# Kernel tuning notes

Hardware: AMD Instinct MI355X
Metric: run time of the kernel (lower is better)

## Reference

```python
import jax, jax.numpy as jnp
import numpy as np

NEG_INF = -9.0e15  # matches torch's -9000000000000000.0 mask value
ALPHA = 0.2        # LeakyReLU negative slope


def setup_inputs() -> dict:
    key = jax.random.key(0)
    k1, k2, k3, k4 = jax.random.split(key, 4)
    N, F_in, F_out = 8192, 128, 128
    x = jax.random.normal(k1, (N, F_in), dtype=jnp.float32)
    adj = jax.random.randint(k2, (N, N), 0, 2, dtype=jnp.int32)
    W = jax.random.normal(k3, (F_in, F_out), dtype=jnp.float32) * (1.0 / np.sqrt(F_in))
    a = jax.random.normal(k4, (2 * F_out, 1), dtype=jnp.float32) * (1.0 / np.sqrt(2 * F_out))
    return {"x": x, "adj": adj, "W": W, "a": a}


def reference(x, adj, W, a):
    # h = W(input): [N, F_out]
    h = x @ W
    F_out = h.shape[1]
    # a([h_i || h_j]) = h_i . a[:F] + h_j . a[F:]  -- identical math to the
    # original NxNx2F concat, without materializing it.
    a_src = a[:F_out, 0]   # coefficients on the row (i) node
    a_dst = a[F_out:, 0]   # coefficients on the column (j) node
    s_src = h @ a_src      # [N]
    s_dst = h @ a_dst      # [N]
    e = jax.nn.leaky_relu(s_src[:, None] + s_dst[None, :], negative_slope=ALPHA)  # [N, N]
    e = jnp.where(adj > 0, e, jnp.float32(NEG_INF))
    attention = jax.nn.softmax(e, axis=1)
    # dropout omitted (identity at eval) for a deterministic baseline
    h_prime = attention @ h  # [N, F_out]
    return h_prime
```

## Files before the change

### kernel.cpp

```cpp
#include <hip/hip_runtime.h>

#define N 8192
#define F 128
#define ALPHA 0.2f

typedef __attribute__((ext_vector_type(8))) short short8;
typedef __attribute__((ext_vector_type(4))) float f32x4;
typedef unsigned short u16;

__device__ __forceinline__ u16 f2bf(float f) {
    unsigned int u = __float_as_uint(f);
    u += 0x7fff + ((u >> 16) & 1);
    return (u16)(u >> 16);
}
__device__ __forceinline__ float bf2f(u16 b) {
    return __uint_as_float(((unsigned int)b) << 16);
}
__device__ __forceinline__ float lrelu(float z) { return fmaxf(z, ALPHA * z); }

__global__ __launch_bounds__(256) void gemm_h(const float* __restrict__ x,
                                              const float* __restrict__ W,
                                              const float* __restrict__ aa,
                                              u16* __restrict__ hT,
                                              float* __restrict__ ssrc,
                                              float* __restrict__ sdst) {
    __shared__ float xs[32 * 128];
    __shared__ float Wsh[32 * 128];
    const int t = threadIdx.x;
    const int i0 = blockIdx.x * 32;
    const int c4 = (t & 31) * 4;
    const int r8 = t >> 5;

#pragma unroll
    for (int p = 0; p < 4; ++p) {
        int rr = p * 8 + r8;
        *(float4*)&xs[rr * 128 + c4] = *(const float4*)&x[(size_t)(i0 + rr) * 128 + c4];
    }

    const int tx = t & 31, ty = t >> 5;
    const int r0 = ty * 4, c0 = tx * 4;
    float acc[4][4] = {};

    for (int kc = 0; kc < 4; ++kc) {
        __syncthreads();
#pragma unroll
        for (int p = 0; p < 4; ++p) {
            int k = p * 8 + r8;
            *(float4*)&Wsh[k * 128 + c4] = *(const float4*)&W[(kc * 32 + k) * 128 + c4];
        }
        __syncthreads();
#pragma unroll 4
        for (int k = 0; k < 32; k += 4) {
            float xr[4][4];
#pragma unroll
            for (int rr = 0; rr < 4; ++rr)
                *(float4*)xr[rr] = *(const float4*)&xs[(r0 + rr) * 128 + kc * 32 + k];
#pragma unroll
            for (int kk = 0; kk < 4; ++kk) {
                float4 wv = *(const float4*)&Wsh[(k + kk) * 128 + c0];
#pragma unroll
                for (int rr = 0; rr < 4; ++rr) {
                    acc[rr][0] += xr[rr][kk] * wv.x;
                    acc[rr][1] += xr[rr][kk] * wv.y;
                    acc[rr][2] += xr[rr][kk] * wv.z;
                    acc[rr][3] += xr[rr][kk] * wv.w;
                }
            }
        }
    }

#pragma unroll
    for (int rr = 0; rr < 4; ++rr)
#pragma unroll
        for (int cc = 0; cc < 4; ++cc)
            hT[(size_t)(c0 + cc) * N + (i0 + r0 + rr)] = f2bf(acc[rr][cc]);

    float4 asv = *(const float4*)&aa[c0];
    float4 adv = *(const float4*)&aa[F + c0];
#pragma unroll
    for (int rr = 0; rr < 4; ++rr) {
        float vs = acc[rr][0] * asv.x + acc[rr][1] * asv.y + acc[rr][2] * asv.z + acc[rr][3] * asv.w;
        float vd = acc[rr][0] * adv.x + acc[rr][1] * adv.y + acc[rr][2] * adv.z + acc[rr][3] * adv.w;
#pragma unroll
        for (int off = 16; off >= 1; off >>= 1) {
            vs += __shfl_down(vs, off, 32);
            vd += __shfl_down(vd, off, 32);
        }
        if (tx == 0) {
            ssrc[i0 + r0 + rr] = vs;
            sdst[i0 + r0 + rr] = vd;
        }
    }
}

__global__ __launch_bounds__(256, 2) void attn_mfma(const int* __restrict__ adj,
                                                    const u16* __restrict__ hT,
                                                    const float* __restrict__ ssrc,
                                                    const float* __restrict__ sdst,
                                                    float* __restrict__ out,
                                                    float* __restrict__ pacc1,
                                                    float* __restrict__ pS) {
    __shared__ short8 wsh[2][4][64];
    __shared__ float srow[2][2][16];

    const int t = threadIdx.x;
    const int w = t >> 6, L = t & 63;
    const int quad = L >> 4, l16 = L & 15;
    const int i0 = blockIdx.x * 32;
    const int split = blockIdx.y;
    const int jbase = split * (N / 2);
    const int NC = (N / 2) / 64;

    const int rt = w & 1, ks = w >> 1;
    const int fragid = rt * 2 + ks;
    const int prow = i0 + rt * 16 + l16;
    const float s_i = ssrc[prow];

    const int* pA = adj + (size_t)prow * N + jbase + ks * 32 + quad * 8;
    const float* pD = sdst + jbase + ks * 32 + quad * 8;
    const u16* pB = hT + (size_t)(w * 32 + l16) * N + jbase + quad * 8;

    f32x4 acc[2][2];
#pragma unroll
    for (int a = 0; a < 2; ++a)
#pragma unroll
        for (int b = 0; b < 2; ++b) acc[a][b] = 0.f;
    float rsum = 0.f;

    auto compute_write = [&](int buf, int4 a0, int4 a1, float4 d0, float4 d1) {
        int m[8] = {a0.x, a0.y, a0.z, a0.w, a1.x, a1.y, a1.z, a1.w};
        float d[8] = {d0.x, d0.y, d0.z, d0.w, d1.x, d1.y, d1.z, d1.w};
        short8 pk;
        float s = 0.f;
#pragma unroll
        for (int k = 0; k < 8; ++k) {
            float e = __expf(lrelu(s_i + d[k]));
            float wv = (m[k] > 0) ? e : 0.f;
            u16 b = f2bf(wv);
            s += bf2f(b);
            pk[k] = (short)b;
        }
        rsum += s;
        wsh[buf][fragid][L] = pk;
    };

    int4 aC0 = *(const int4*)(pA);
    int4 aC1 = *(const int4*)(pA + 4);
    float4 dC0 = *(const float4*)(pD);
    float4 dC1 = *(const float4*)(pD + 4);
    compute_write(0, aC0, aC1, dC0, dC1);

    short8 Bbuf[2][2];
#pragma unroll
    for (int c2 = 0; c2 < 2; ++c2)
#pragma unroll
        for (int kb = 0; kb < 2; ++kb)
            Bbuf[c2][kb] = *(const short8*)(pB + (size_t)c2 * 16 * N + kb * 32);

    int4 aN0 = *(const int4*)(pA + 64);
    int4 aN1 = *(const int4*)(pA + 64 + 4);
    float4 dN0 = *(const float4*)(pD + 64);
    float4 dN1 = *(const float4*)(pD + 64 + 4);

    for (int c = 1; c < NC; ++c) {
        __syncthreads();
        const int coff = c * 64;

        short8 Bload[2][2];
#pragma unroll
        for (int c2 = 0; c2 < 2; ++c2)
#pragma unroll
            for (int kb = 0; kb < 2; ++kb)
                Bload[c2][kb] = *(const short8*)(pB + (size_t)c2 * 16 * N + kb * 32 + coff);

        const int cn = (c + 1 < NC) ? c + 1 : NC - 1;
        int4 aP0 = *(const int4*)(pA + cn * 64);
        int4 aP1 = *(const int4*)(pA + cn * 64 + 4);
        float4 dP0 = *(const float4*)(pD + cn * 64);
        float4 dP1 = *(const float4*)(pD + cn * 64 + 4);

        short8 af[4];
#pragma unroll
        for (int fs = 0; fs < 4; ++fs) af[fs] = wsh[(c - 1) & 1][fs][L];
#pragma unroll
        for (int c2 = 0; c2 < 2; ++c2)
#pragma unroll
            for (int rc = 0; rc < 2; ++rc)
#pragma unroll
                for (int kb = 0; kb < 2; ++kb)
                    acc[c2][rc] = __builtin_amdgcn_mfma_f32_16x16x32_bf16(
                        af[rc * 2 + kb], Bbuf[c2][kb], acc[c2][rc], 0, 0, 0);

        compute_write(c & 1, aN0, aN1, dN0, dN1);

        aN0 = aP0; aN1 = aP1; dN0 = dP0; dN1 = dP1;
#pragma unroll
        for (int c2 = 0; c2 < 2; ++c2)
#pragma unroll
            for (int kb = 0; kb < 2; ++kb) Bbuf[c2][kb] = Bload[c2][kb];
    }

    __syncthreads();
    {
        short8 af[4];
#pragma unroll
        for (int fs = 0; fs < 4; ++fs) af[fs] = wsh[(NC - 1) & 1][fs][L];
#pragma unroll
        for (int c2 = 0; c2 < 2; ++c2)
#pragma unroll
            for (int rc = 0; rc < 2; ++rc)
#pragma unroll
                for (int kb = 0; kb < 2; ++kb)
                    acc[c2][rc] = __builtin_amdgcn_mfma_f32_16x16x32_bf16(
                        af[rc * 2 + kb], Bbuf[c2][kb], acc[c2][rc], 0, 0, 0);
    }

    float* dst = split ? pacc1 : out;
#pragma unroll
    for (int c2 = 0; c2 < 2; ++c2) {
        const int col = (w * 2 + c2) * 16 + l16;
#pragma unroll
        for (int rc = 0; rc < 2; ++rc) {
            const int row0 = i0 + rc * 16 + quad * 4;
#pragma unroll
            for (int r = 0; r < 4; ++r)
                dst[(size_t)(row0 + r) * F + col] = acc[c2][rc][r];
        }
    }

    rsum += __shfl_xor(rsum, 16);
    rsum += __shfl_xor(rsum, 32);
    if (L < 16) srow[rt][ks][l16] = rsum;
    __syncthreads();
    if (t < 32) pS[split * N + i0 + t] = srow[t >> 4][0][t & 15] + srow[t >> 4][1][t & 15];
}

__global__ __launch_bounds__(256) void finalize(float* __restrict__ out,
                                                const float* __restrict__ pacc1,
                                                const float* __restrict__ pS) {
    const int idx = (blockIdx.x * 256 + threadIdx.x) * 4;
    const int i = idx >> 7;
    const float inv = 1.0f / (pS[i] + pS[N + i]);
    float4 a0 = *(const float4*)&out[idx];
    float4 a1 = *(const float4*)&pacc1[idx];
    float4 o = {(a0.x + a1.x) * inv, (a0.y + a1.y) * inv,
                (a0.z + a1.z) * inv, (a0.w + a1.w) * inv};
    *(float4*)&out[idx] = o;
}

extern "C" void kernel_launch(void* const* d_in, const int* in_sizes, int n_in,
                              void* d_out, int out_size, void* d_ws, size_t ws_size,
                              hipStream_t stream) {
    (void)in_sizes; (void)n_in; (void)out_size; (void)ws_size;
    const float* x   = (const float*)d_in[0];
    const int*   adj = (const int*)d_in[1];
    const float* W   = (const float*)d_in[2];
    const float* a   = (const float*)d_in[3];
    float* out = (float*)d_out;

    u16* hT     = (u16*)d_ws;
    float* ssrc = (float*)(hT + (size_t)N * F);
    float* sdst = ssrc + N;
    float* pS   = sdst + N;
    float* pacc1 = pS + 2 * N;

    gemm_h<<<N / 32, 256, 0, stream>>>(x, W, a, hT, ssrc, sdst);
    attn_mfma<<<dim3(N / 32, 2), 256, 0, stream>>>(adj, hT, ssrc, sdst, out, pacc1, pS);
    finalize<<<(N * F / 4) / 256, 256, 0, stream>>>(out, pacc1, pS);
}
```

Measured before the change: 413.4 us.

## Restructure attention kernel: per-wave row tiles, 8-way key split, no LDS

The attention kernel is rewritten so each wave owns 16 rows and all 128 output columns. Each wave computes its own bf16 attention weights in registers and feeds them straight into MFMA, which removes the shared-memory staging and block barriers. The key dimension is split 8 ways instead of 2, and occupancy is raised to 4 blocks per SM, with a two-deep register prefetch of adj and sdst. In exchange, finalize must now reduce 8 partial accumulators, which adds workspace traffic, and each wave re-reads the hT tiles that were previously shared across the block.

```diff
diff --git a/kernel.cpp b/kernel.cpp
--- a/kernel.cpp
+++ b/kernel.cpp
@@ -2,6 +2,10 @@
 
 #define N 8192
 #define F 128
+#define NS 8
+#define JC (N / NS)
+#define CK 32
+#define NC (JC / CK)
 #define ALPHA 0.2f
 
 typedef __attribute__((ext_vector_type(8))) short short8;
@@ -93,158 +97,118 @@
     }
 }
 
-__global__ __launch_bounds__(256, 2) void attn_mfma(const int* __restrict__ adj,
+__global__ __launch_bounds__(256, 4) void attn_mfma(const int* __restrict__ adj,
                                                     const u16* __restrict__ hT,
                                                     const float* __restrict__ ssrc,
                                                     const float* __restrict__ sdst,
-                                                    float* __restrict__ out,
-                                                    float* __restrict__ pacc1,
+                                                    float* __restrict__ pacc,
                                                     float* __restrict__ pS) {
-    __shared__ short8 wsh[2][4][64];
-    __shared__ float srow[2][2][16];
-
     const int t = threadIdx.x;
     const int w = t >> 6, L = t & 63;
     const int quad = L >> 4, l16 = L & 15;
-    const int i0 = blockIdx.x * 32;
+    const int i0 = blockIdx.x * 64 + w * 16;
     const int split = blockIdx.y;
-    const int jbase = split * (N / 2);
-    const int NC = (N / 2) / 64;
-
-    const int rt = w & 1, ks = w >> 1;
-    const int fragid = rt * 2 + ks;
-    const int prow = i0 + rt * 16 + l16;
-    const float s_i = ssrc[prow];
-
-    const int* pA = adj + (size_t)prow * N + jbase + ks * 32 + quad * 8;
-    const float* pD = sdst + jbase + ks * 32 + quad * 8;
-    const u16* pB = hT + (size_t)(w * 32 + l16) * N + jbase + quad * 8;
-
-    f32x4 acc[2][2];
-#pragma unroll
-    for (int a = 0; a < 2; ++a)
-#pragma unroll
-        for (int b = 0; b < 2; ++b) acc[a][b] = 0.f;
+    const int jbase = split * JC;
+
+    const int row = i0 + l16;
+    const float s_i = ssrc[row];
+    const int* pA = adj + (size_t)row * N + jbase + quad * 8;
+    const float* pD = sdst + jbase + quad * 8;
+    const u16* pB = hT + (size_t)l16 * N + jbase + quad * 8;
+
+    f32x4 acc[8];
+#pragma unroll
+    for (int cg = 0; cg < 8; ++cg) acc[cg] = 0.f;
     float rsum = 0.f;
 
-    auto compute_write = [&](int buf, int4 a0, int4 a1, float4 d0, float4 d1) {
-        int m[8] = {a0.x, a0.y, a0.z, a0.w, a1.x, a1.y, a1.z, a1.w};
-        float d[8] = {d0.x, d0.y, d0.z, d0.w, d1.x, d1.y, d1.z, d1.w};
-        short8 pk;
-        float s = 0.f;
-#pragma unroll
-        for (int k = 0; k < 8; ++k) {
-            float e = __expf(lrelu(s_i + d[k]));
-            float wv = (m[k] > 0) ? e : 0.f;
-            u16 b = f2bf(wv);
-            s += bf2f(b);
-            pk[k] = (short)b;
-        }
-        rsum += s;
-        wsh[buf][fragid][L] = pk;
-    };
-
-    int4 aC0 = *(const int4*)(pA);
-    int4 aC1 = *(const int4*)(pA + 4);
-    float4 dC0 = *(const float4*)(pD);
-    float4 dC1 = *(const float4*)(pD + 4);
-    compute_write(0, aC0, aC1, dC0, dC1);
-
-    short8 Bbuf[2][2];
-#pragma unroll
-    for (int c2 = 0; c2 < 2; ++c2)
-#pragma unroll
-        for (int kb = 0; kb < 2; ++kb)
-            Bbuf[c2][kb] = *(const short8*)(pB + (size_t)c2 * 16 * N + kb * 32);
-
-    int4 aN0 = *(const int4*)(pA + 64);
-    int4 aN1 = *(const int4*)(pA + 64 + 4);
-    float4 dN0 = *(const float4*)(pD + 64);
-    float4 dN1 = *(const float4*)(pD + 64 + 4);
-
-    for (int c = 1; c < NC; ++c) {
-        __syncthreads();
-        const int coff = c * 64;
-
-        short8 Bload[2][2];
-#pragma unroll
-        for (int c2 = 0; c2 < 2; ++c2)
-#pragma unroll
-            for (int kb = 0; kb < 2; ++kb)
-                Bload[c2][kb] = *(const short8*)(pB + (size_t)c2 * 16 * N + kb * 32 + coff);
-
-        const int cn = (c + 1 < NC) ? c + 1 : NC - 1;
-        int4 aP0 = *(const int4*)(pA + cn * 64);
-        int4 aP1 = *(const int4*)(pA + cn * 64 + 4);
-        float4 dP0 = *(const float4*)(pD + cn * 64);
-        float4 dP1 = *(const float4*)(pD + cn * 64 + 4);
-
-        short8 af[4];
-#pragma unroll
-        for (int fs = 0; fs < 4; ++fs) af[fs] = wsh[(c - 1) & 1][fs][L];
-#pragma unroll
-        for (int c2 = 0; c2 < 2; ++c2)
-#pragma unroll
-            for (int rc = 0; rc < 2; ++rc)
-#pragma unroll
-                for (int kb = 0; kb < 2; ++kb)
-                    acc[c2][rc] = __builtin_amdgcn_mfma_f32_16x16x32_bf16(
-                        af[rc * 2 + kb], Bbuf[c2][kb], acc[c2][rc], 0, 0, 0);
-
-        compute_write(c & 1, aN0, aN1, dN0, dN1);
-
-        aN0 = aP0; aN1 = aP1; dN0 = dP0; dN1 = dP1;
-#pragma unroll
-        for (int c2 = 0; c2 < 2; ++c2)
-#pragma unroll
-            for (int kb = 0; kb < 2; ++kb) Bbuf[c2][kb] = Bload[c2][kb];
-    }
-
-    __syncthreads();
-    {
-        short8 af[4];
-#pragma unroll
-        for (int fs = 0; fs < 4; ++fs) af[fs] = wsh[(NC - 1) & 1][fs][L];
-#pragma unroll
-        for (int c2 = 0; c2 < 2; ++c2)
-#pragma unroll
-            for (int rc = 0; rc < 2; ++rc)
-#pragma unroll
-                for (int kb = 0; kb < 2; ++kb)
-                    acc[c2][rc] = __builtin_amdgcn_mfma_f32_16x16x32_bf16(
-                        af[rc * 2 + kb], Bbuf[c2][kb], acc[c2][rc], 0, 0, 0);
-    }
-
-    float* dst = split ? pacc1 : out;
-#pragma unroll
-    for (int c2 = 0; c2 < 2; ++c2) {
-        const int col = (w * 2 + c2) * 16 + l16;
-#pragma unroll
-        for (int rc = 0; rc < 2; ++rc) {
-            const int row0 = i0 + rc * 16 + quad * 4;
-#pragma unroll
-            for (int r = 0; r < 4; ++r)
-                dst[(size_t)(row0 + r) * F + col] = acc[c2][rc][r];
-        }
+    int4 aj[2][2];
+    float4 sd[2][2];
+    aj[0][0] = *(const int4*)(pA);
+    aj[0][1] = *(const int4*)(pA + 4);
+    sd[0][0] = *(const float4*)(pD);
+    sd[0][1] = *(const float4*)(pD + 4);
+    aj[1][0] = *(const int4*)(pA + CK);
+    aj[1][1] = *(const int4*)(pA + CK + 4);
+    sd[1][0] = *(const float4*)(pD + CK);
+    sd[1][1] = *(const float4*)(pD + CK + 4);
+
+#pragma unroll 2
+    for (int c = 0; c < NC; ++c) {
+        const int s = c & 1;
+        const int off = c * CK;
+
+        short8 B0[4];
+#pragma unroll
+        for (int cg = 0; cg < 4; ++cg)
+            B0[cg] = *(const short8*)(pB + (size_t)cg * 16 * N + off);
+
+        short8 wf;
+        {
+            int m[8] = {aj[s][0].x, aj[s][0].y, aj[s][0].z, aj[s][0].w,
+                        aj[s][1].x, aj[s][1].y, aj[s][1].z, aj[s][1].w};
+            float d[8] = {sd[s][0].x, sd[s][0].y, sd[s][0].z, sd[s][0].w,
+                          sd[s][1].x, sd[s][1].y, sd[s][1].z, sd[s][1].w};
+#pragma unroll
+            for (int k = 0; k < 8; ++k) {
+                float e = __expf(lrelu(s_i + d[k]));
+                float wv = (m[k] > 0) ? e : 0.f;
+                u16 b = f2bf(wv);
+                rsum += bf2f(b);
+                wf[k] = (short)b;
+            }
+        }
+
+        const int cp = (c + 2 < NC) ? c + 2 : c;
+        const int offp = cp * CK;
+        aj[s][0] = *(const int4*)(pA + offp);
+        aj[s][1] = *(const int4*)(pA + offp + 4);
+        sd[s][0] = *(const float4*)(pD + offp);
+        sd[s][1] = *(const float4*)(pD + offp + 4);
+
+        short8 B1[4];
+#pragma unroll
+        for (int cg = 0; cg < 4; ++cg)
+            B1[cg] = *(const short8*)(pB + (size_t)(cg + 4) * 16 * N + off);
+
+#pragma unroll
+        for (int cg = 0; cg < 4; ++cg)
+            acc[cg] = __builtin_amdgcn_mfma_f32_16x16x32_bf16(wf, B0[cg], acc[cg], 0, 0, 0);
+#pragma unroll
+        for (int cg = 0; cg < 4; ++cg)
+            acc[cg + 4] = __builtin_amdgcn_mfma_f32_16x16x32_bf16(wf, B1[cg], acc[cg + 4], 0, 0, 0);
+    }
+
+    float* dst = pacc + (size_t)split * N * F;
+#pragma unroll
+    for (int cg = 0; cg < 8; ++cg) {
+        const int col = cg * 16 + l16;
+        const int r0 = i0 + quad * 4;
+#pragma unroll
+        for (int r = 0; r < 4; ++r)
+            dst[(size_t)(r0 + r) * F + col] = acc[cg][r];
     }
 
     rsum += __shfl_xor(rsum, 16);
     rsum += __shfl_xor(rsum, 32);
-    if (L < 16) srow[rt][ks][l16] = rsum;
-    __syncthreads();
-    if (t < 32) pS[split * N + i0 + t] = srow[t >> 4][0][t & 15] + srow[t >> 4][1][t & 15];
+    if (L < 16) pS[(size_t)split * N + i0 + l16] = rsum;
 }
 
 __global__ __launch_bounds__(256) void finalize(float* __restrict__ out,
-                                                const float* __restrict__ pacc1,
+                                                const float* __restrict__ pacc,
                                                 const float* __restrict__ pS) {
     const int idx = (blockIdx.x * 256 + threadIdx.x) * 4;
     const int i = idx >> 7;
-    const float inv = 1.0f / (pS[i] + pS[N + i]);
-    float4 a0 = *(const float4*)&out[idx];
-    float4 a1 = *(const float4*)&pacc1[idx];
-    float4 o = {(a0.x + a1.x) * inv, (a0.y + a1.y) * inv,
-                (a0.z + a1.z) * inv, (a0.w + a1.w) * inv};
+    float s = 0.f;
+#pragma unroll
+    for (int k = 0; k < NS; ++k) s += pS[(size_t)k * N + i];
+    float4 a = {0.f, 0.f, 0.f, 0.f};
+#pragma unroll
+    for (int k = 0; k < NS; ++k) {
+        float4 v = *(const float4*)&pacc[(size_t)k * N * F + idx];
+        a.x += v.x; a.y += v.y; a.z += v.z; a.w += v.w;
+    }
+    const float inv = 1.0f / s;
+    float4 o = {a.x * inv, a.y * inv, a.z * inv, a.w * inv};
     *(float4*)&out[idx] = o;
 }
 
@@ -262,9 +226,9 @@
     float* ssrc = (float*)(hT + (size_t)N * F);
     float* sdst = ssrc + N;
     float* pS   = sdst + N;
-    float* pacc1 = pS + 2 * N;
+    float* pacc = pS + (size_t)NS * N;
 
     gemm_h<<<N / 32, 256, 0, stream>>>(x, W, a, hT, ssrc, sdst);
-    attn_mfma<<<dim3(N / 32, 2), 256, 0, stream>>>(adj, hT, ssrc, sdst, out, pacc1, pS);
-    finalize<<<(N * F / 4) / 256, 256, 0, stream>>>(out, pacc1, pS);
-}
+    attn_mfma<<<dim3(N / 64, NS), 256, 0, stream>>>(adj, hT, ssrc, sdst, pacc, pS);
+    finalize<<<(N * F / 4) / 256, 256, 0, stream>>>(out, pacc, pS);
+}
```

After: 509.2 us. +23.2%, slower.
